# Kernel tuning notes

Hardware: AMD Instinct MI355X
Metric: run time of the kernel (lower is better)

The kernel has to match this reference:

```python
import jax, jax.numpy as jnp
import numpy as np

B, S, E, D, A, V, EM, T = 128, 196, 2048, 512, 256, 10000, 512, 20


def setup_inputs() -> dict:
    key = jax.random.key(0)
    ks = jax.random.split(key, 16)
    def rn(k, shape, scale=0.02):
        return jax.random.normal(k, shape, dtype=jnp.float32) * scale
    return {
        "encoder_features": jax.random.normal(ks[0], (B, S, E), dtype=jnp.float32),
        "captions": jax.random.randint(ks[1], (B, T), 0, V),
        "emb_table": rn(ks[2], (V, EM)),
        "W_ea": rn(ks[3], (E, A)), "b_ea": jnp.zeros((A,), jnp.float32),
        "W_da": rn(ks[4], (D, A)), "b_da": jnp.zeros((A,), jnp.float32),
        "W_fa": rn(ks[5], (A, 1)), "b_fa": jnp.zeros((1,), jnp.float32),
        "W_ih": rn(ks[6], (EM + E, 4 * D)), "b_ih": jnp.zeros((4 * D,), jnp.float32),
        "W_hh": rn(ks[7], (D, 4 * D)), "b_hh": jnp.zeros((4 * D,), jnp.float32),
        "W_cp": rn(ks[8], (E, EM)), "b_cp": jnp.zeros((EM,), jnp.float32),
        "W_hp": rn(ks[9], (D, EM)), "b_hp": jnp.zeros((EM,), jnp.float32),
        "W_op": rn(ks[10], (EM, V)), "b_op": jnp.zeros((V,), jnp.float32),
        "W_inith": rn(ks[11], (E, D)), "b_inith": jnp.zeros((D,), jnp.float32),
        "W_initc": rn(ks[12], (E, D)), "b_initc": jnp.zeros((D,), jnp.float32),
    }


def reference(encoder_features, captions, emb_table, W_ea, b_ea, W_da, b_da,
              W_fa, b_fa, W_ih, b_ih, W_hh, b_hh, W_cp, b_cp, W_hp, b_hp,
              W_op, b_op, W_inith, b_inith, W_initc, b_initc):
    # init LSTM state from mean-pooled encoder features
    mean_feat = encoder_features.mean(axis=1)            # [B, E]
    h0 = mean_feat @ W_inith + b_inith                   # [B, D]
    c0 = mean_feat @ W_initc + b_initc                   # [B, D]
    # encoder branch of Bahdanau attention is step-invariant: precompute
    enc_att = jnp.einsum('bse,ea->bsa', encoder_features, W_ea) + b_ea  # [B, S, A]
    embs = emb_table[captions]                           # [B, T, EM]
    xs = jnp.swapaxes(embs, 0, 1)                        # [T, B, EM]

    def step(carry, x_t):
        h, c = carry
        # Bahdanau: relu(enc_att + dec_att) -> score -> softmax -> context
        dec_att = h @ W_da + b_da                        # [B, A]
        combined = jax.nn.relu(enc_att + dec_att[:, None, :])  # [B, S, A]
        scores = (combined @ W_fa)[..., 0] + b_fa[0]     # [B, S]
        alpha = jax.nn.softmax(scores, axis=1)           # [B, S]
        context = jnp.einsum('bs,bse->be', alpha, encoder_features)  # [B, E]
        # LSTMCell on [embedding; context]
        x_in = jnp.concatenate([x_t, context], axis=-1)  # [B, EM+E]
        gates = x_in @ W_ih + b_ih + h @ W_hh + b_hh     # [B, 4D]
        i, f, g, o = jnp.split(gates, 4, axis=-1)
        c_new = jax.nn.sigmoid(f) * c + jax.nn.sigmoid(i) * jnp.tanh(g)
        h_new = jax.nn.sigmoid(o) * jnp.tanh(c_new)
        # output: proj(context) + proj(hidden) -> vocab logits (dropout = eval identity)
        feat = context @ W_cp + b_cp + h_new @ W_hp + b_hp  # [B, EM]
        logits = feat @ W_op + b_op                      # [B, V]
        return (h_new, c_new), logits

    _, logits = jax.lax.scan(step, (h0, c0), xs)         # [T, B, V]
    return jnp.swapaxes(logits, 0, 1)                    # [B, T, V]
```

## Files before the change

kernel.cpp:

```cpp
#include <hip/hip_runtime.h>
#include <hip/hip_bf16.h>

#define B 128
#define S 196
#define E 2048
#define D 512
#define A 256
#define V 10000
#define EM 512
#define T 20
#define KCAT 2560

typedef unsigned short u16;
typedef __bf16 bf16x8 __attribute__((ext_vector_type(8)));
typedef float f32x4 __attribute__((ext_vector_type(4)));
typedef u16 u16x8 __attribute__((ext_vector_type(8)));
typedef u16 u16x4 __attribute__((ext_vector_type(4)));

__device__ inline u16 f2bf(float f) {
    union { float f; unsigned u; } x; x.f = f;
    return (u16)((x.u + 0x7FFFu + ((x.u >> 16) & 1u)) >> 16);
}
__device__ inline float bf2f(u16 h) {
    union { unsigned u; float f; } x; x.u = ((unsigned)h) << 16;
    return x.f;
}
__device__ inline bf16x8 ld_bf8(const u16* p) {
    return __builtin_bit_cast(bf16x8, *reinterpret_cast<const u16x8*>(p));
}
__device__ inline bf16x8 cvt_bf8(const float* p) {
    float4 u = *reinterpret_cast<const float4*>(p);
    float4 v = *reinterpret_cast<const float4*>(p + 4);
    u16x8 t;
    t[0] = f2bf(u.x); t[1] = f2bf(u.y); t[2] = f2bf(u.z); t[3] = f2bf(u.w);
    t[4] = f2bf(v.x); t[5] = f2bf(v.y); t[6] = f2bf(v.z); t[7] = f2bf(v.w);
    return __builtin_bit_cast(bf16x8, t);
}
__device__ inline float sigm(float x) { return 1.f / (1.f + expf(-x)); }

struct PairT {
    const void* Ap;
    long lda;
    const u16* Bt;
    long ldb;
    int K;
};

template <int NP, bool AF32, typename OutT, int WTM, int WTN, int WVM, int WVN>
__global__ __launch_bounds__(WVM * WVN * 64) void gemm_mfma(
    int N, PairT q0, PairT q1, PairT q2,
    const float* __restrict__ bias1, const float* __restrict__ bias2,
    OutT* __restrict__ Cc, long ldc)
{
    const int tid  = threadIdx.x;
    const int w    = tid >> 6;
    const int lane = tid & 63;
    const int lr   = lane & 15;
    const int lg   = lane >> 4;
    const int mrow = blockIdx.y * (WVM * WTM * 16) + (w / WVN) * (WTM * 16);
    const int ncol = blockIdx.x * (WVN * WTN * 16) + (w % WVN) * (WTN * 16);

    f32x4 acc[WTM][WTN];
#pragma unroll
    for (int i = 0; i < WTM; ++i)
#pragma unroll
        for (int j = 0; j < WTN; ++j) acc[i][j] = (f32x4){0.f, 0.f, 0.f, 0.f};

    const PairT qs[3] = {q0, q1, q2};
#pragma unroll
    for (int p = 0; p < NP; ++p) {
        const PairT pp = qs[p];
        const int nk = pp.K >> 5;
        const u16*   Ab = (const u16*)pp.Ap;
        const float* Af = (const float*)pp.Ap;
        size_t aoff[WTM];
#pragma unroll
        for (int mi = 0; mi < WTM; ++mi)
            aoff[mi] = (size_t)(mrow + mi * 16 + lr) * pp.lda + lg * 8;
        const u16* Bp = pp.Bt + (size_t)(ncol + lr) * pp.ldb + lg * 8;

#pragma unroll 2
        for (int kk = 0; kk < nk; ++kk) {
            const int ko = kk * 32;
            bf16x8 av[WTM], bv[WTN];
#pragma unroll
            for (int mi = 0; mi < WTM; ++mi) {
                if (AF32) av[mi] = cvt_bf8(Af + aoff[mi] + ko);
                else      av[mi] = ld_bf8(Ab + aoff[mi] + ko);
            }
#pragma unroll
            for (int ni = 0; ni < WTN; ++ni)
                bv[ni] = ld_bf8(Bp + ko + (size_t)(ni * 16) * pp.ldb);
#pragma unroll
            for (int mi = 0; mi < WTM; ++mi)
#pragma unroll
                for (int ni = 0; ni < WTN; ++ni)
                    acc[mi][ni] = __builtin_amdgcn_mfma_f32_16x16x32_bf16(
                        av[mi], bv[ni], acc[mi][ni], 0, 0, 0);
        }
    }

#pragma unroll
    for (int ni = 0; ni < WTN; ++ni) {
        const int col = ncol + ni * 16 + lr;
        if (col >= N) continue;
        float bs = 0.f;
        if (bias1) bs += bias1[col];
        if (bias2) bs += bias2[col];
#pragma unroll
        for (int mi = 0; mi < WTM; ++mi) {
#pragma unroll
            for (int r = 0; r < 4; ++r) {
                const int row = mrow + mi * 16 + lg * 4 + r;
                const float v = acc[mi][ni][r] + bs;
                if constexpr (sizeof(OutT) == 2)
                    Cc[(size_t)row * ldc + col] = (OutT)f2bf(v);
                else
                    Cc[(size_t)row * ldc + col] = v;
            }
        }
    }
}

__global__ __launch_bounds__(256) void init_xin_h(
    const u16* __restrict__ h_cur, u16* __restrict__ xin)
{
    const int idx = blockIdx.x * 256 + threadIdx.x;
    const int b = idx >> 9;
    const int d = idx & (D - 1);
    xin[(size_t)b * KCAT + 2048 + d] = h_cur[idx];
}

template <bool FBF>
__global__ __launch_bounds__(256) void alpha_ctx_lstm(
    const void* __restrict__ Fv,
    const u16*  __restrict__ enc,
    const u16*  __restrict__ W_daT,
    const float* __restrict__ b_da,
    const float* __restrict__ W_fa,
    const float* __restrict__ b_ih_,
    const float* __restrict__ b_hh_,
    const float* __restrict__ egates,
    const float* __restrict__ part,
    const float* __restrict__ c_rd,
    float* __restrict__ c_wr,
    const u16*  __restrict__ h0,
    u16* __restrict__ h_all,
    u16* __restrict__ ctx_all,
    u16* __restrict__ xin,
    int t)
{
    const int blk  = blockIdx.x;
    const int tid  = threadIdx.x;
    const int w    = tid >> 6;
    const int lane = tid & 63;
    const int b    = blk >> 1;
    const int q    = blk & 1;

    __shared__ float hl[D];
    __shared__ float dec[A];
    __shared__ float wfa[A];
    __shared__ float sc[S];
    __shared__ float red[8];

    if (t == 0) {
        hl[tid]       = bf2f(h0[b * D + tid]);
        hl[tid + 256] = bf2f(h0[b * D + 256 + tid]);
    } else {
        const int tt = t - 1;
#pragma unroll
        for (int half = 0; half < 2; ++half) {
            const int d = tid + half * 256;
            float g4[4];
#pragma unroll
            for (int g = 0; g < 4; ++g) {
                const int col = ((d >> 4) << 6) + (g << 4) + (d & 15);
                float s = b_ih_[g * D + d] + b_hh_[g * D + d] +
                          egates[((size_t)(b * T + tt) << 11) + col];
#pragma unroll
                for (int z = 0; z < 4; ++z)
                    s += part[((size_t)(z * B + b) << 11) + col];
                g4[g] = s;
            }
            const int idx = (b << 9) + d;
            const float cn = sigm(g4[1]) * c_rd[idx] + sigm(g4[0]) * tanhf(g4[2]);
            const float hf = sigm(g4[3]) * tanhf(cn);
            hl[d] = hf;
            if (q == 0) {
                c_wr[idx] = cn;
                const u16 hv = f2bf(hf);
                h_all[((size_t)(b * T + tt)) * D + d] = hv;
                xin[(size_t)b * KCAT + 2048 + d] = hv;
            }
        }
    }
    wfa[tid] = W_fa[tid];
    __syncthreads();

    {
        float acc = 0.f;
        const u16* wr = W_daT + (size_t)tid * D;
#pragma unroll 4
        for (int i = 0; i < D / 8; ++i) {
            const u16x8 v = *reinterpret_cast<const u16x8*>(wr + i * 8);
#pragma unroll
            for (int j = 0; j < 8; ++j) acc += bf2f(v[j]) * hl[i * 8 + j];
        }
        dec[tid] = acc + b_da[tid];
    }
    __syncthreads();

    if (tid < S) {
        const u16* er = enc + ((size_t)b * S + tid) * A;
        float v = 0.f;
#pragma unroll 4
        for (int i = 0; i < A / 8; ++i) {
            const u16x8 e8 = *reinterpret_cast<const u16x8*>(er + i * 8);
#pragma unroll
            for (int j = 0; j < 8; ++j) {
                float x = bf2f(e8[j]) + dec[i * 8 + j];
                x = x > 0.f ? x : 0.f;
                v += x * wfa[i * 8 + j];
            }
        }
        sc[tid] = v;
    }
    __syncthreads();

    float m = -1e30f;
    for (int s = tid; s < S; s += 256) m = fmaxf(m, sc[s]);
    for (int off = 32; off; off >>= 1) m = fmaxf(m, __shfl_down(m, off));
    if (lane == 0) red[w] = m;
    __syncthreads();
    if (tid == 0) red[0] = fmaxf(fmaxf(red[0], red[1]), fmaxf(red[2], red[3]));
    __syncthreads();
    m = red[0];

    float sum = 0.f;
    for (int s = tid; s < S; s += 256) {
        const float ev = __expf(sc[s] - m);
        sc[s] = ev;
        sum += ev;
    }
    for (int off = 32; off; off >>= 1) sum += __shfl_down(sum, off);
    if (lane == 0) red[4 + w] = sum;
    __syncthreads();
    if (tid == 0) red[4] = red[4] + red[5] + red[6] + red[7];
    __syncthreads();
    const float inv = 1.f / red[4];

    {
        const int e0 = q * 1024 + tid * 4;
        float a0 = 0.f, a1 = 0.f, a2 = 0.f, a3 = 0.f;
        float d0 = 0.f, d1 = 0.f, d2 = 0.f, d3 = 0.f;
        if (FBF) {
            const u16* Fb  = (const u16*)Fv + (size_t)b * S * E + e0;
            const u16* Fb2 = Fb + (size_t)98 * E;
#pragma unroll 7
            for (int s = 0; s < 98; ++s) {
                const u16x4 v1 = *reinterpret_cast<const u16x4*>(Fb + (size_t)s * E);
                const u16x4 v2 = *reinterpret_cast<const u16x4*>(Fb2 + (size_t)s * E);
                const float al1 = sc[s];
                const float al2 = sc[s + 98];
                a0 += al1 * bf2f(v1[0]); a1 += al1 * bf2f(v1[1]);
                a2 += al1 * bf2f(v1[2]); a3 += al1 * bf2f(v1[3]);
                d0 += al2 * bf2f(v2[0]); d1 += al2 * bf2f(v2[1]);
                d2 += al2 * bf2f(v2[2]); d3 += al2 * bf2f(v2[3]);
            }
        } else {
            const float* Ff  = (const float*)Fv + (size_t)b * S * E + e0;
            const float* Ff2 = Ff + (size_t)98 * E;
#pragma unroll 7
            for (int s = 0; s < 98; ++s) {
                const float4 u = *reinterpret_cast<const float4*>(Ff + (size_t)s * E);
                const float4 v = *reinterpret_cast<const float4*>(Ff2 + (size_t)s * E);
                const float al1 = sc[s];
                const float al2 = sc[s + 98];
                a0 += al1 * u.x; a1 += al1 * u.y; a2 += al1 * u.z; a3 += al1 * u.w;
                d0 += al2 * v.x; d1 += al2 * v.y; d2 += al2 * v.z; d3 += al2 * v.w;
            }
        }
        a0 += d0; a1 += d1; a2 += d2; a3 += d3;
        u16x4 o;
        o[0] = f2bf(a0 * inv); o[1] = f2bf(a1 * inv);
        o[2] = f2bf(a2 * inv); o[3] = f2bf(a3 * inv);
        *reinterpret_cast<u16x4*>(ctx_all + ((size_t)(b * T + t)) * E + e0) = o;
        *reinterpret_cast<u16x4*>(xin + (size_t)b * KCAT + e0) = o;
    }
}

__global__ __launch_bounds__(128) void gates_split4(
    const u16* __restrict__ xin, const u16* __restrict__ W_chT,
    float* __restrict__ part)
{
    const int tid  = threadIdx.x;
    const int w    = tid >> 6;
    const int lane = tid & 63;
    const int lr   = lane & 15;
    const int lg   = lane >> 4;
    const int mrow = blockIdx.y * 16;
    const int ncol = blockIdx.x * 128 + w * 64;
    const int z    = blockIdx.z;
    const int kb   = z * 640;

    f32x4 acc[4];
#pragma unroll
    for (int j = 0; j < 4; ++j) acc[j] = (f32x4){0.f, 0.f, 0.f, 0.f};

    const u16* Ap = xin + (size_t)(mrow + lr) * KCAT + kb + lg * 8;
    const u16* Bp = W_chT + (size_t)(ncol + lr) * KCAT + kb + lg * 8;

#pragma unroll 4
    for (int kk = 0; kk < 20; ++kk) {
        const int ko = kk * 32;
        const bf16x8 av = ld_bf8(Ap + ko);
        bf16x8 bv[4];
#pragma unroll
        for (int ni = 0; ni < 4; ++ni)
            bv[ni] = ld_bf8(Bp + ko + (size_t)(ni * 16) * KCAT);
#pragma unroll
        for (int ni = 0; ni < 4; ++ni)
            acc[ni] = __builtin_amdgcn_mfma_f32_16x16x32_bf16(av, bv[ni], acc[ni], 0, 0, 0);
    }

#pragma unroll
    for (int ni = 0; ni < 4; ++ni) {
        const int col = ncol + ni * 16 + lr;
#pragma unroll
        for (int r = 0; r < 4; ++r) {
            const int row = mrow + lg * 4 + r;
            part[((size_t)(z * B + row) << 11) + col] = acc[ni][r];
        }
    }
}

__global__ __launch_bounds__(256) void lstm_last(
    const float* __restrict__ part,
    const float* __restrict__ egates,
    const float* __restrict__ b_ih_, const float* __restrict__ b_hh_,
    const float* __restrict__ c_rd,
    u16* __restrict__ h_all)
{
    const int idx = blockIdx.x * 256 + threadIdx.x;
    const int b = idx >> 9;
    const int d = idx & (D - 1);
    const int tt = T - 1;
    float g4[4];
#pragma unroll
    for (int g = 0; g < 4; ++g) {
        const int col = ((d >> 4) << 6) + (g << 4) + (d & 15);
        float s = b_ih_[g * D + d] + b_hh_[g * D + d] +
                  egates[((size_t)(b * T + tt) << 11) + col];
#pragma unroll
        for (int z = 0; z < 4; ++z)
            s += part[((size_t)(z * B + b) << 11) + col];
        g4[g] = s;
    }
    const float cn = sigm(g4[1]) * c_rd[idx] + sigm(g4[0]) * tanhf(g4[2]);
    h_all[((size_t)(b * T + tt)) * D + d] = f2bf(sigm(g4[3]) * tanhf(cn));
}

__global__ __launch_bounds__(256) void transpose_bf(
    const float* __restrict__ in, int K, int N, u16* __restrict__ out)
{
    __shared__ float tls[32][33];
    const int k0 = blockIdx.y * 32, n0 = blockIdx.x * 32;
    const int c = threadIdx.x & 31, r8 = threadIdx.x >> 5;
#pragma unroll
    for (int i = 0; i < 4; ++i) {
        const int k = r8 + i * 8;
        float v = 0.f;
        if (n0 + c < N) v = in[(size_t)(k0 + k) * N + n0 + c];
        tls[k][c] = v;
    }
    __syncthreads();
#pragma unroll
    for (int i = 0; i < 4; ++i) {
        const int n = r8 + i * 8;
        out[(size_t)(n0 + n) * K + k0 + c] = f2bf(tls[c][n]);
    }
}

__global__ __launch_bounds__(256) void transpose_bf_gates(
    const float* __restrict__ in, int Kin, u16* __restrict__ out, int ldo, int ko)
{
    __shared__ float tls[32][33];
    const int k0 = blockIdx.y * 32, n0 = blockIdx.x * 32;
    const int c = threadIdx.x & 31, r8 = threadIdx.x >> 5;
#pragma unroll
    for (int i = 0; i < 4; ++i) {
        const int k = r8 + i * 8;
        tls[k][c] = in[(size_t)(k0 + k) * 2048 + n0 + c];
    }
    __syncthreads();
#pragma unroll
    for (int i = 0; i < 4; ++i) {
        const int nn = r8 + i * 8;
        const int n = n0 + nn;
        const int g = n >> 9, d = n & (D - 1);
        const int orow = ((d >> 4) << 6) + (g << 4) + (d & 15);
        out[(size_t)orow * ldo + ko + k0 + c] = f2bf(tls[c][nn]);
    }
}

template <bool WRITE>
__global__ __launch_bounds__(256) void conv_mean(
    const float* __restrict__ F, u16* __restrict__ Fbf, u16* __restrict__ meanbf)
{
    const int idx = blockIdx.x * 256 + threadIdx.x;
    const int b = idx >> 11;
    const int e = idx & (E - 1);
    const float* src = F + (size_t)b * S * E + e;
    float acc = 0.f;
#pragma unroll 2
    for (int s = 0; s < S; ++s) {
        const float v = src[(size_t)s * E];
        acc += v;
        if (WRITE) Fbf[(size_t)b * S * E + (size_t)s * E + e] = f2bf(v);
    }
    meanbf[idx] = f2bf(acc * (1.f / (float)S));
}

__global__ __launch_bounds__(256) void gather_embs_bf(
    const int* __restrict__ captions, const float* __restrict__ table,
    u16* __restrict__ out)
{
    const int idx = blockIdx.x * 256 + threadIdx.x;
    const int row = idx >> 6;
    const int ch  = idx & 63;
    const int cap = captions[row];
    const float* src = table + (size_t)cap * EM + ch * 8;
    float4 u = *reinterpret_cast<const float4*>(src);
    float4 v = *reinterpret_cast<const float4*>(src + 4);
    u16x8 t;
    t[0] = f2bf(u.x); t[1] = f2bf(u.y); t[2] = f2bf(u.z); t[3] = f2bf(u.w);
    t[4] = f2bf(v.x); t[5] = f2bf(v.y); t[6] = f2bf(v.z); t[7] = f2bf(v.w);
    *reinterpret_cast<u16x8*>(out + (size_t)row * EM + ch * 8) = t;
}

struct Pair {
    const float* Aptr; int lda; const float* Wptr; int ldw; int K;
};

template <int NP>
__global__ __launch_bounds__(256) void gemm_f32(
    int M, int N, Pair p0, Pair p1, Pair p2,
    const float* __restrict__ bias1, const float* __restrict__ bias2,
    float* __restrict__ C, long ldc)
{
    __shared__ float As[64][17];
    __shared__ float Ws[16][64];
    const int tid = threadIdx.x;
    const int row0 = blockIdx.y * 64, col0 = blockIdx.x * 64;
    const int tx = tid & 15, ty = tid >> 4;
    float acc[4][4] = {};
    Pair ps[3] = {p0, p1, p2};
#pragma unroll
    for (int p = 0; p < NP; ++p) {
        const float* Ag = ps[p].Aptr; const float* Wg = ps[p].Wptr;
        const int lda = ps[p].lda, ldw = ps[p].ldw, K = ps[p].K;
        for (int k0 = 0; k0 < K; k0 += 16) {
            {
                const int k = tid & 15, mb = tid >> 4;
#pragma unroll
                for (int i = 0; i < 4; ++i) {
                    const int m = mb + 16 * i, gr = row0 + m;
                    float v = 0.f;
                    if (gr < M) v = Ag[(size_t)gr * lda + k0 + k];
                    As[m][k] = v;
                }
            }
            {
                const int n = tid & 63, kb = tid >> 6, gc = col0 + n;
#pragma unroll
                for (int i = 0; i < 4; ++i) {
                    const int k = kb * 4 + i;
                    float v = 0.f;
                    if (gc < N) v = Wg[(size_t)(k0 + k) * ldw + gc];
                    Ws[k][n] = v;
                }
            }
            __syncthreads();
#pragma unroll
            for (int k = 0; k < 16; ++k) {
                float av[4];
#pragma unroll
                for (int i = 0; i < 4; ++i) av[i] = As[ty * 4 + i][k];
                const float4 bv = reinterpret_cast<const float4*>(&Ws[k][0])[tx];
                const float bvv[4] = {bv.x, bv.y, bv.z, bv.w};
#pragma unroll
                for (int i = 0; i < 4; ++i)
#pragma unroll
                    for (int j = 0; j < 4; ++j) acc[i][j] += av[i] * bvv[j];
            }
            __syncthreads();
        }
    }
#pragma unroll
    for (int i = 0; i < 4; ++i) {
        const int r = row0 + ty * 4 + i;
        if (r >= M) continue;
#pragma unroll
        for (int j = 0; j < 4; ++j) {
            const int cidx = col0 + tx * 4 + j;
            if (cidx >= N) continue;
            float v = acc[i][j];
            if (bias1) v += bias1[cidx];
            if (bias2) v += bias2[cidx];
            C[(size_t)r * ldc + cidx] = v;
        }
    }
}

__global__ __launch_bounds__(256) void mean_pool(const float* __restrict__ F,
                                                 float* __restrict__ mean)
{
    const int idx = blockIdx.x * 256 + threadIdx.x;
    const int b = idx >> 11, e = idx & (E - 1);
    const float* Fb = F + (size_t)b * S * E + e;
    float acc = 0.f;
    for (int s = 0; s < S; ++s) acc += Fb[(size_t)s * E];
    mean[idx] = acc * (1.f / (float)S);
}

__global__ __launch_bounds__(256) void gather_embs(const int* __restrict__ captions,
                                                   const float* __restrict__ table,
                                                   float* __restrict__ out)
{
    const int idx = blockIdx.x * 256 + threadIdx.x;
    const int per_row = EM / 4;
    const int row = idx / per_row;
    const int col = idx - row * per_row;
    const int cap = captions[row];
    reinterpret_cast<float4*>(out)[idx] =
        reinterpret_cast<const float4*>(table + (size_t)cap * EM)[col];
}

__global__ __launch_bounds__(256) void attn_softmax(
    const float* __restrict__ enc_att, const float* __restrict__ dec_att,
    const float* __restrict__ W_fa, const float* __restrict__ b_fa,
    float* __restrict__ alpha)
{
    const int b = blockIdx.x, tid = threadIdx.x;
    const int wave = tid >> 6, lane = tid & 63;
    __shared__ float dec[A], wfa[A], sc[S], redm[4], reds[4];
    dec[tid] = dec_att[b * A + tid];
    wfa[tid] = W_fa[tid];
    __syncthreads();
    for (int s = wave; s < S; s += 4) {
        const float* ea = enc_att + ((size_t)b * S + s) * A;
        float v = 0.f;
#pragma unroll
        for (int i = 0; i < 4; ++i) {
            const int a = lane + 64 * i;
            float x = ea[a] + dec[a];
            x = x > 0.f ? x : 0.f;
            v += x * wfa[a];
        }
        for (int off = 32; off; off >>= 1) v += __shfl_down(v, off);
        if (lane == 0) sc[s] = v + b_fa[0];
    }
    __syncthreads();
    float m = -1e30f;
    for (int s = tid; s < S; s += 256) m = fmaxf(m, sc[s]);
    for (int off = 32; off; off >>= 1) m = fmaxf(m, __shfl_down(m, off));
    if (lane == 0) redm[wave] = m;
    __syncthreads();
    if (tid == 0) redm[0] = fmaxf(fmaxf(redm[0], redm[1]), fmaxf(redm[2], redm[3]));
    __syncthreads();
    m = redm[0];
    float sum = 0.f;
    for (int s = tid; s < S; s += 256) {
        const float ev = expf(sc[s] - m);
        sc[s] = ev; sum += ev;
    }
    for (int off = 32; off; off >>= 1) sum += __shfl_down(sum, off);
    if (lane == 0) reds[wave] = sum;
    __syncthreads();
    if (tid == 0) reds[0] = reds[0] + reds[1] + reds[2] + reds[3];
    __syncthreads();
    const float inv = 1.f / reds[0];
    for (int s = tid; s < S; s += 256) alpha[b * S + s] = sc[s] * inv;
}

__global__ __launch_bounds__(256) void context_kernel(
    const float* __restrict__ F, const float* __restrict__ alpha,
    float* __restrict__ ctx)
{
    const int chunks = E / 256;
    const int b = blockIdx.x / chunks;
    const int ec = blockIdx.x - b * chunks;
    const int e = ec * 256 + threadIdx.x;
    __shared__ float al[S];
    for (int s = threadIdx.x; s < S; s += 256) al[s] = alpha[b * S + s];
    __syncthreads();
    const float* Fb = F + (size_t)b * S * E + e;
    float acc = 0.f;
    for (int s = 0; s < S; ++s) acc += al[s] * Fb[(size_t)s * E];
    ctx[b * E + e] = acc;
}

__global__ __launch_bounds__(256) void lstm_cell(
    const float* __restrict__ gates, float* __restrict__ h, float* __restrict__ c)
{
    const int idx = blockIdx.x * 256 + threadIdx.x;
    const int b = idx >> 9, d = idx & (D - 1);
    const float* g = gates + (size_t)b * 4 * D;
    const float gi = g[d], gf = g[D + d], gg = g[2 * D + d], go = g[3 * D + d];
    const float cn = sigm(gf) * c[idx] + sigm(gi) * tanhf(gg);
    c[idx] = cn;
    h[idx] = sigm(go) * tanhf(cn);
}

extern "C" void kernel_launch(void* const* d_in, const int* in_sizes, int n_in,
                              void* d_out, int out_size, void* d_ws, size_t ws_size,
                              hipStream_t stream)
{
    const float* F        = (const float*)d_in[0];
    const int*   captions = (const int*)  d_in[1];
    const float* table    = (const float*)d_in[2];
    const float* W_ea     = (const float*)d_in[3];
    const float* b_ea     = (const float*)d_in[4];
    const float* W_da     = (const float*)d_in[5];
    const float* b_da     = (const float*)d_in[6];
    const float* W_fa     = (const float*)d_in[7];
    const float* b_fa     = (const float*)d_in[8];
    const float* W_ih     = (const float*)d_in[9];
    const float* b_ih     = (const float*)d_in[10];
    const float* W_hh     = (const float*)d_in[11];
    const float* b_hh     = (const float*)d_in[12];
    const float* W_cp     = (const float*)d_in[13];
    const float* b_cp     = (const float*)d_in[14];
    const float* W_hp     = (const float*)d_in[15];
    const float* b_hp     = (const float*)d_in[16];
    const float* W_op     = (const float*)d_in[17];
    const float* b_op     = (const float*)d_in[18];
    const float* W_inith  = (const float*)d_in[19];
    const float* b_inith  = (const float*)d_in[20];
    const float* W_initc  = (const float*)d_in[21];
    const float* b_initc  = (const float*)d_in[22];

    float* out = (float*)d_out;
    const int VP2 = 10240;

    char* base = (char*)d_ws;
    size_t off = 0;
    auto alloc = [&](size_t bytes) -> void* {
        off = (off + 255) & ~(size_t)255;
        void* p = base + off;
        off += bytes;
        return p;
    };

    u16* W_eaT    = (u16*)alloc((size_t)A * E * 2);
    u16* W_daT    = (u16*)alloc((size_t)A * D * 2);
    u16* W_iheT   = (u16*)alloc((size_t)2048 * EM * 2);
    u16* W_chT    = (u16*)alloc((size_t)2048 * KCAT * 2);
    u16* W_cpT    = (u16*)alloc((size_t)EM * E * 2);
    u16* W_hpT    = (u16*)alloc((size_t)EM * D * 2);
    u16* W_opT    = (u16*)alloc((size_t)VP2 * EM * 2);
    u16* W_inithT = (u16*)alloc((size_t)D * E * 2);
    u16* W_initcT = (u16*)alloc((size_t)D * E * 2);
    u16* embs     = (u16*)alloc((size_t)B * T * EM * 2);
    u16* mean_bf  = (u16*)alloc((size_t)B * E * 2);
    u16* h_cur    = (u16*)alloc((size_t)B * D * 2);
    u16* h_all    = (u16*)alloc((size_t)B * T * D * 2);
    u16* ctx_all  = (u16*)alloc((size_t)B * T * E * 2);
    u16* xin      = (u16*)alloc((size_t)B * KCAT * 2);
    u16* feat_all = (u16*)alloc((size_t)B * T * EM * 2);
    u16* enc_bf   = (u16*)alloc((size_t)B * S * A * 2);
    float* cbuf0  = (float*)alloc((size_t)B * D * 4);
    float* cbuf1  = (float*)alloc((size_t)B * D * 4);
    float* egates = (float*)alloc((size_t)B * T * 2048 * 4);
    float* part   = (float*)alloc((size_t)4 * B * 2048 * 4);
    const size_t need_base = off;
    u16* F_bf     = (u16*)alloc((size_t)B * S * E * 2);
    const size_t need_fbf = off;

    const bool ok_base = need_base <= ws_size;
    const bool ok_fbf  = need_fbf <= ws_size;

    if (!ok_base) {
        float* ws = (float*)d_ws;
        float* mean_feat = ws;  ws += B * E;
        float* h         = ws;  ws += B * D;
        float* c         = ws;  ws += B * D;
        float* enc_att   = ws;  ws += (size_t)B * S * A;
        float* fembs     = ws;  ws += (size_t)B * T * EM;
        float* fdec      = ws;  ws += B * A;
        float* falpha    = ws;  ws += B * S;
        float* fctx      = ws;  ws += B * E;
        float* fgates    = ws;  ws += B * 4 * D;
        float* ffeat     = ws;  ws += B * EM;
        const Pair ZP = {nullptr, 0, nullptr, 0, 0};
        mean_pool<<<(B * E) / 256, 256, 0, stream>>>(F, mean_feat);
        { Pair p = {mean_feat, E, W_inith, D, E};
          gemm_f32<1><<<dim3(D / 64, B / 64), 256, 0, stream>>>(B, D, p, ZP, ZP, b_inith, nullptr, h, D); }
        { Pair p = {mean_feat, E, W_initc, D, E};
          gemm_f32<1><<<dim3(D / 64, B / 64), 256, 0, stream>>>(B, D, p, ZP, ZP, b_initc, nullptr, c, D); }
        { Pair p = {F, E, W_ea, A, E};
          gemm_f32<1><<<dim3(A / 64, (B * S) / 64), 256, 0, stream>>>(B * S, A, p, ZP, ZP, b_ea, nullptr, enc_att, A); }
        gather_embs<<<(B * T * (EM / 4)) / 256, 256, 0, stream>>>(captions, table, fembs);
        for (int t = 0; t < T; ++t) {
            { Pair p = {h, D, W_da, A, D};
              gemm_f32<1><<<dim3(A / 64, B / 64), 256, 0, stream>>>(B, A, p, ZP, ZP, b_da, nullptr, fdec, A); }
            attn_softmax<<<B, 256, 0, stream>>>(enc_att, fdec, W_fa, b_fa, falpha);
            context_kernel<<<B * (E / 256), 256, 0, stream>>>(F, falpha, fctx);
            { Pair p0 = {fembs + (size_t)t * EM, T * EM, W_ih, 4 * D, EM};
              Pair p1 = {fctx, E, W_ih + (size_t)EM * 4 * D, 4 * D, E};
              Pair p2 = {h, D, W_hh, 4 * D, D};
              gemm_f32<3><<<dim3((4 * D) / 64, B / 64), 256, 0, stream>>>(B, 4 * D, p0, p1, p2, b_ih, b_hh, fgates, 4 * D); }
            lstm_cell<<<(B * D) / 256, 256, 0, stream>>>(fgates, h, c);
            { Pair p0 = {fctx, E, W_cp, EM, E};
              Pair p1 = {h, D, W_hp, EM, D};
              gemm_f32<2><<<dim3(EM / 64, B / 64), 256, 0, stream>>>(B, EM, p0, p1, ZP, b_cp, b_hp, ffeat, EM); }
            { Pair p = {ffeat, EM, W_op, V, EM};
              gemm_f32<1><<<dim3((V + 63) / 64, B / 64), 256, 0, stream>>>(B, V, p, ZP, ZP, b_op, nullptr, out + (size_t)t * V, (long)T * V); }
        }
        return;
    }

    const PairT ZP = {nullptr, 0, nullptr, 0, 0};

    transpose_bf<<<dim3(A / 32, E / 32), 256, 0, stream>>>(W_ea, E, A, W_eaT);
    transpose_bf<<<dim3(A / 32, D / 32), 256, 0, stream>>>(W_da, D, A, W_daT);
    transpose_bf_gates<<<dim3(64, EM / 32), 256, 0, stream>>>(W_ih, EM, W_iheT, EM, 0);
    transpose_bf_gates<<<dim3(64, E / 32), 256, 0, stream>>>(W_ih + (size_t)EM * 2048, E, W_chT, KCAT, 0);
    transpose_bf_gates<<<dim3(64, D / 32), 256, 0, stream>>>(W_hh, D, W_chT, KCAT, 2048);
    transpose_bf<<<dim3(EM / 32, E / 32), 256, 0, stream>>>(W_cp, E, EM, W_cpT);
    transpose_bf<<<dim3(EM / 32, D / 32), 256, 0, stream>>>(W_hp, D, EM, W_hpT);
    transpose_bf<<<dim3(VP2 / 32, EM / 32), 256, 0, stream>>>(W_op, EM, V, W_opT);
    transpose_bf<<<dim3(D / 32, E / 32), 256, 0, stream>>>(W_inith, E, D, W_inithT);
    transpose_bf<<<dim3(D / 32, E / 32), 256, 0, stream>>>(W_initc, E, D, W_initcT);

    if (ok_fbf)
        conv_mean<true><<<(B * E) / 256, 256, 0, stream>>>(F, F_bf, mean_bf);
    else
        conv_mean<false><<<(B * E) / 256, 256, 0, stream>>>(F, nullptr, mean_bf);

    gather_embs_bf<<<(B * T * (EM / 8)) / 256, 256, 0, stream>>>(captions, table, embs);

    { PairT p = {mean_bf, E, W_inithT, E, E};
      gemm_mfma<1, false, u16, 2, 4, 1, 4><<<dim3(2, 4), 256, 0, stream>>>(
          D, p, ZP, ZP, b_inith, nullptr, h_cur, D); }
    { PairT p = {mean_bf, E, W_initcT, E, E};
      gemm_mfma<1, false, float, 2, 4, 1, 4><<<dim3(2, 4), 256, 0, stream>>>(
          D, p, ZP, ZP, b_initc, nullptr, cbuf1, D); }

    init_xin_h<<<(B * D) / 256, 256, 0, stream>>>(h_cur, xin);

    if (ok_fbf) {
        PairT p = {F_bf, E, W_eaT, E, E};
        gemm_mfma<1, false, u16, 4, 4, 1, 4><<<dim3(1, (B * S) / 64), 256, 0, stream>>>(
            A, p, ZP, ZP, b_ea, nullptr, enc_bf, A);
    } else {
        PairT p = {F, E, W_eaT, E, E};
        gemm_mfma<1, true, u16, 4, 4, 1, 4><<<dim3(1, (B * S) / 64), 256, 0, stream>>>(
            A, p, ZP, ZP, b_ea, nullptr, enc_bf, A);
    }

    { PairT p = {embs, EM, W_iheT, EM, EM};
      gemm_mfma<1, false, float, 2, 4, 2, 2><<<dim3(16, 40), 256, 0, stream>>>(
          2048, p, ZP, ZP, nullptr, nullptr, egates, 2048); }

    for (int t = 0; t < T; ++t) {
        const int tt = t - 1;
        const float* crd = (tt >= 0 && (tt & 1)) ? cbuf0 : cbuf1;
        float*       cwr = (tt >= 0 && (tt & 1)) ? cbuf1 : cbuf0;

        if (ok_fbf)
            alpha_ctx_lstm<true><<<256, 256, 0, stream>>>(
                F_bf, enc_bf, W_daT, b_da, W_fa, b_ih, b_hh, egates, part,
                crd, cwr, h_cur, h_all, ctx_all, xin, t);
        else
            alpha_ctx_lstm<false><<<256, 256, 0, stream>>>(
                F, enc_bf, W_daT, b_da, W_fa, b_ih, b_hh, egates, part,
                crd, cwr, h_cur, h_all, ctx_all, xin, t);

        gates_split4<<<dim3(16, 8, 4), 128, 0, stream>>>(xin, W_chT, part);
    }

    lstm_last<<<(B * D) / 256, 256, 0, stream>>>(
        part, egates, b_ih, b_hh, ((T - 1) & 1) ? cbuf0 : cbuf1, h_all);

    { PairT p0 = {ctx_all, E, W_cpT, E, E};
      PairT p1 = {h_all, D, W_hpT, D, D};
      gemm_mfma<2, false, u16, 1, 4, 2, 2><<<dim3(EM / 128, (B * T) / 32), 256, 0, stream>>>(
          EM, p0, p1, ZP, b_cp, b_hp, feat_all, EM); }

    { PairT p = {feat_all, EM, W_opT, EM, EM};
      gemm_mfma<1, false, float, 4, 4, 2, 2><<<dim3(VP2 / 128, (B * T) / 128), 256, 0, stream>>>(
          V, p, ZP, ZP, b_op, nullptr, out, V); }
}
```

Baseline: 1.540 ms.

## Add LDS-tiled encoder-attention GEMM, split gates K eight ways, widen context ILP

Adds a dedicated 128x128 LDS-tiled MFMA GEMM with XOR-swizzled shared memory for the encoder-attention projection, replacing the generic kernel on the bf16 path. The recurrent gates GEMM now splits K into eight slices instead of four, giving twice as many blocks per step. The LSTM combine and lstm_last therefore sum eight partial buffers, and the partial buffer doubles in size. The context reduction uses four independent accumulator streams over S instead of two, giving more loads in flight. The cost is extra partial-sum traffic and a larger workspace.

New measurement: 1.543 ms. No clear change (+0.2%).

```diff
diff --git a/kernel.cpp b/kernel.cpp
--- a/kernel.cpp
+++ b/kernel.cpp
@@ -117,6 +117,104 @@
                     Cc[(size_t)row * ldc + col] = (OutT)f2bf(v);
                 else
                     Cc[(size_t)row * ldc + col] = v;
+            }
+        }
+    }
+}
+
+__global__ __launch_bounds__(256) void gemm_enc(
+    const u16* __restrict__ Abf,
+    const u16* __restrict__ Bt,
+    const float* __restrict__ bias,
+    u16* __restrict__ Cc)
+{
+    __shared__ u16 As[128 * 64];
+    __shared__ u16 Bs[128 * 64];
+
+    const int tid  = threadIdx.x;
+    const int w    = tid >> 6;
+    const int lane = tid & 63;
+    const int lr   = lane & 15;
+    const int lg   = lane >> 4;
+    const int brow = blockIdx.y * 128;
+    const int bcol = blockIdx.x * 128;
+    const int wrow = (w >> 1) * 64;
+    const int wcol = (w & 1) * 64;
+
+    int arow[4], acb[4], aphys[4];
+#pragma unroll
+    for (int i = 0; i < 4; ++i) {
+        const int s = (tid + 256 * i) * 16;
+        arow[i]  = s >> 7;
+        acb[i]   = s & 127;
+        aphys[i] = (s ^ ((arow[i] & 7) << 4)) >> 1;
+    }
+
+    int aoff[2][4], boff[2][4];
+#pragma unroll
+    for (int kh = 0; kh < 2; ++kh) {
+#pragma unroll
+        for (int i = 0; i < 4; ++i) {
+            const int ra = wrow + i * 16 + lr;
+            aoff[kh][i] = (((ra << 7) + (kh << 6) + (lg << 4)) ^ ((ra & 7) << 4)) >> 1;
+            const int rb = wcol + i * 16 + lr;
+            boff[kh][i] = (((rb << 7) + (kh << 6) + (lg << 4)) ^ ((rb & 7) << 4)) >> 1;
+        }
+    }
+
+    f32x4 acc[4][4];
+#pragma unroll
+    for (int i = 0; i < 4; ++i)
+#pragma unroll
+        for (int j = 0; j < 4; ++j) acc[i][j] = (f32x4){0.f, 0.f, 0.f, 0.f};
+
+    for (int k0 = 0; k0 < 2048; k0 += 64) {
+        u16x8 av[4], bv[4];
+#pragma unroll
+        for (int i = 0; i < 4; ++i) {
+            av[i] = *reinterpret_cast<const u16x8*>(
+                Abf + (size_t)(brow + arow[i]) * 2048 + k0 + (acb[i] >> 1));
+            bv[i] = *reinterpret_cast<const u16x8*>(
+                Bt + (size_t)(bcol + arow[i]) * 2048 + k0 + (acb[i] >> 1));
+        }
+        __syncthreads();
+#pragma unroll
+        for (int i = 0; i < 4; ++i) {
+            *reinterpret_cast<u16x8*>(As + aphys[i]) = av[i];
+            *reinterpret_cast<u16x8*>(Bs + aphys[i]) = bv[i];
+        }
+        __syncthreads();
+
+#pragma unroll
+        for (int kh = 0; kh < 2; ++kh) {
+            bf16x8 af[4], bf_[4];
+#pragma unroll
+            for (int mi = 0; mi < 4; ++mi)
+                af[mi] = __builtin_bit_cast(bf16x8,
+                    *reinterpret_cast<const u16x8*>(As + aoff[kh][mi]));
+#pragma unroll
+            for (int ni = 0; ni < 4; ++ni)
+                bf_[ni] = __builtin_bit_cast(bf16x8,
+                    *reinterpret_cast<const u16x8*>(Bs + boff[kh][ni]));
+#pragma unroll
+            for (int mi = 0; mi < 4; ++mi)
+#pragma unroll
+                for (int ni = 0; ni < 4; ++ni)
+                    acc[mi][ni] = __builtin_amdgcn_mfma_f32_16x16x32_bf16(
+                        af[mi], bf_[ni], acc[mi][ni], 0, 0, 0);
+        }
+    }
+
+#pragma unroll
+    for (int ni = 0; ni < 4; ++ni) {
+        const int col = bcol + wcol + ni * 16 + lr;
+        const float bs = bias[col];
+#pragma unroll
+        for (int mi = 0; mi < 4; ++mi) {
+#pragma unroll
+            for (int r = 0; r < 4; ++r) {
+                const int row = brow + wrow + mi * 16 + lg * 4 + r;
+                Cc[(size_t)row * 256 + col] = f2bf(acc[mi][ni][r] + bs);
             }
         }
     }
@@ -178,7 +276,7 @@
                 float s = b_ih_[g * D + d] + b_hh_[g * D + d] +
                           egates[((size_t)(b * T + tt) << 11) + col];
 #pragma unroll
-                for (int z = 0; z < 4; ++z)
+                for (int z = 0; z < 8; ++z)
                     s += part[((size_t)(z * B + b) << 11) + col];
                 g4[g] = s;
             }
@@ -252,35 +350,50 @@
     {
         const int e0 = q * 1024 + tid * 4;
         float a0 = 0.f, a1 = 0.f, a2 = 0.f, a3 = 0.f;
+        float b0 = 0.f, b1 = 0.f, b2 = 0.f, b3 = 0.f;
+        float c0 = 0.f, c1 = 0.f, c2 = 0.f, c3 = 0.f;
         float d0 = 0.f, d1 = 0.f, d2 = 0.f, d3 = 0.f;
         if (FBF) {
-            const u16* Fb  = (const u16*)Fv + (size_t)b * S * E + e0;
-            const u16* Fb2 = Fb + (size_t)98 * E;
+            const u16* F0 = (const u16*)Fv + (size_t)b * S * E + e0;
+            const u16* F1 = F0 + (size_t)49 * E;
+            const u16* F2 = F0 + (size_t)98 * E;
+            const u16* F3 = F0 + (size_t)147 * E;
 #pragma unroll 7
-            for (int s = 0; s < 98; ++s) {
-                const u16x4 v1 = *reinterpret_cast<const u16x4*>(Fb + (size_t)s * E);
-                const u16x4 v2 = *reinterpret_cast<const u16x4*>(Fb2 + (size_t)s * E);
-                const float al1 = sc[s];
-                const float al2 = sc[s + 98];
-                a0 += al1 * bf2f(v1[0]); a1 += al1 * bf2f(v1[1]);
-                a2 += al1 * bf2f(v1[2]); a3 += al1 * bf2f(v1[3]);
-                d0 += al2 * bf2f(v2[0]); d1 += al2 * bf2f(v2[1]);
-                d2 += al2 * bf2f(v2[2]); d3 += al2 * bf2f(v2[3]);
+            for (int s = 0; s < 49; ++s) {
+                const u16x4 v0 = *reinterpret_cast<const u16x4*>(F0 + (size_t)s * E);
+                const u16x4 v1 = *reinterpret_cast<const u16x4*>(F1 + (size_t)s * E);
+                const u16x4 v2 = *reinterpret_cast<const u16x4*>(F2 + (size_t)s * E);
+                const u16x4 v3 = *reinterpret_cast<const u16x4*>(F3 + (size_t)s * E);
+                const float l0 = sc[s], l1 = sc[s + 49], l2 = sc[s + 98], l3 = sc[s + 147];
+                a0 += l0 * bf2f(v0[0]); a1 += l0 * bf2f(v0[1]);
+                a2 += l0 * bf2f(v0[2]); a3 += l0 * bf2f(v0[3]);
+                b0 += l1 * bf2f(v1[0]); b1 += l1 * bf2f(v1[1]);
+                b2 += l1 * bf2f(v1[2]); b3 += l1 * bf2f(v1[3]);
+                c0 += l2 * bf2f(v2[0]); c1 += l2 * bf2f(v2[1]);
+                c2 += l2 * bf2f(v2[2]); c3 += l2 * bf2f(v2[3]);
+                d0 += l3 * bf2f(v3[0]); d1 += l3 * bf2f(v3[1]);
+                d2 += l3 * bf2f(v3[2]); d3 += l3 * bf2f(v3[3]);
             }
         } else {
-            const float* Ff  = (const float*)Fv + (size_t)b * S * E + e0;
-            const float* Ff2 = Ff + (size_t)98 * E;
+            const float* F0 = (const float*)Fv + (size_t)b * S * E + e0;
+            const float* F1 = F0 + (size_t)49 * E;
+            const float* F2 = F0 + (size_t)98 * E;
+            const float* F3 = F0 + (size_t)147 * E;
 #pragma unroll 7
-            for (int s = 0; s < 98; ++s) {
-                const float4 u = *reinterpret_cast<const float4*>(Ff + (size_t)s * E);
-                const float4 v = *reinterpret_cast<const float4*>(Ff2 + (size_t)s * E);
-                const float al1 = sc[s];
-                const float al2 = sc[s + 98];
-                a0 += al1 * u.x; a1 += al1 * u.y; a2 += al1 * u.z; a3 += al1 * u.w;
-                d0 += al2 * v.x; d1 += al2 * v.y; d2 += al2 * v.z; d3 += al2 * v.w;
-            }
-        }
-        a0 += d0; a1 += d1; a2 += d2; a3 += d3;
+            for (int s = 0; s < 49; ++s) {
+                const float4 v0 = *reinterpret_cast<const float4*>(F0 + (size_t)s * E);
+                const float4 v1 = *reinterpret_cast<const float4*>(F1 + (size_t)s * E);
+                const float4 v2 = *reinterpret_cast<const float4*>(F2 + (size_t)s * E);
+                const float4 v3 = *reinterpret_cast<const float4*>(F3 + (size_t)s * E);
+                const float l0 = sc[s], l1 = sc[s + 49], l2 = sc[s + 98], l3 = sc[s + 147];
+                a0 += l0 * v0.x; a1 += l0 * v0.y; a2 += l0 * v0.z; a3 += l0 * v0.w;
+                b0 += l1 * v1.x; b1 += l1 * v1.y; b2 += l1 * v1.z; b3 += l1 * v1.w;
+                c0 += l2 * v2.x; c1 += l2 * v2.y; c2 += l2 * v2.z; c3 += l2 * v2.w;
+                d0 += l3 * v3.x; d1 += l3 * v3.y; d2 += l3 * v3.z; d3 += l3 * v3.w;
+            }
+        }
+        a0 += b0 + c0 + d0; a1 += b1 + c1 + d1;
+        a2 += b2 + c2 + d2; a3 += b3 + c3 + d3;
         u16x4 o;
         o[0] = f2bf(a0 * inv); o[1] = f2bf(a1 * inv);
         o[2] = f2bf(a2 * inv); o[3] = f2bf(a3 * inv);
@@ -289,7 +402,7 @@
     }
 }
 
-__global__ __launch_bounds__(128) void gates_split4(
+__global__ __launch_bounds__(128) void gates_split8(
     const u16* __restrict__ xin, const u16* __restrict__ W_chT,
     float* __restrict__ part)
 {
@@ -301,7 +414,7 @@
     const int mrow = blockIdx.y * 16;
     const int ncol = blockIdx.x * 128 + w * 64;
     const int z    = blockIdx.z;
-    const int kb   = z * 640;
+    const int kb   = z * 320;
 
     f32x4 acc[4];
 #pragma unroll
@@ -310,8 +423,8 @@
     const u16* Ap = xin + (size_t)(mrow + lr) * KCAT + kb + lg * 8;
     const u16* Bp = W_chT + (size_t)(ncol + lr) * KCAT + kb + lg * 8;
 
-#pragma unroll 4
-    for (int kk = 0; kk < 20; ++kk) {
+#pragma unroll
+    for (int kk = 0; kk < 10; ++kk) {
         const int ko = kk * 32;
         const bf16x8 av = ld_bf8(Ap + ko);
         bf16x8 bv[4];
@@ -352,7 +465,7 @@
         float s = b_ih_[g * D + d] + b_hh_[g * D + d] +
                   egates[((size_t)(b * T + tt) << 11) + col];
 #pragma unroll
-        for (int z = 0; z < 4; ++z)
+        for (int z = 0; z < 8; ++z)
             s += part[((size_t)(z * B + b) << 11) + col];
         g4[g] = s;
     }
@@ -672,7 +785,7 @@
     float* cbuf0  = (float*)alloc((size_t)B * D * 4);
     float* cbuf1  = (float*)alloc((size_t)B * D * 4);
     float* egates = (float*)alloc((size_t)B * T * 2048 * 4);
-    float* part   = (float*)alloc((size_t)4 * B * 2048 * 4);
+    float* part   = (float*)alloc((size_t)8 * B * 2048 * 4);
     const size_t need_base = off;
     u16* F_bf     = (u16*)alloc((size_t)B * S * E * 2);
     const size_t need_fbf = off;
@@ -750,9 +863,7 @@
     init_xin_h<<<(B * D) / 256, 256, 0, stream>>>(h_cur, xin);
 
     if (ok_fbf) {
-        PairT p = {F_bf, E, W_eaT, E, E};
-        gemm_mfma<1, false, u16, 4, 4, 1, 4><<<dim3(1, (B * S) / 64), 256, 0, stream>>>(
-            A, p, ZP, ZP, b_ea, nullptr, enc_bf, A);
+        gemm_enc<<<dim3(2, (B * S) / 128), 256, 0, stream>>>(F_bf, W_eaT, b_ea, enc_bf);
     } else {
         PairT p = {F, E, W_eaT, E, E};
         gemm_mfma<1, true, u16, 4, 4, 1, 4><<<dim3(1, (B * S) / 64), 256, 0, stream>>>(
@@ -777,7 +888,7 @@
                 F, enc_bf, W_daT, b_da, W_fa, b_ih, b_hh, egates, part,
                 crd, cwr, h_cur, h_all, ctx_all, xin, t);
 
-        gates_split4<<<dim3(16, 8, 4), 128, 0, stream>>>(xin, W_chT, part);
+        gates_split8<<<dim3(16, 8, 8), 128, 0, stream>>>(xin, W_chT, part);
     }
 
     lstm_last<<<(B * D) / 256, 256, 0, stream>>>(
```
